# Optimization experiments

Hardware: AMD Instinct MI355X
Metric: run time of the kernel (lower is better)

## Reference

```python
import jax, jax.numpy as jnp
import numpy as np

BATCH, IN_DIM, OUT_DIM, DEGREE = 4096, 1024, 1024, 7


def setup_inputs() -> dict:
    key = jax.random.key(0)
    k1, k2 = jax.random.split(key)
    std = 1.0 / (IN_DIM * (DEGREE + 1))
    return {
        "x": jax.random.normal(k1, (BATCH, IN_DIM), dtype=jnp.float32),
        "a": jnp.zeros((1,), dtype=jnp.float32),
        "q": jnp.ones((1,), dtype=jnp.float32),
        "coeffs": jax.random.normal(k2, (IN_DIM, OUT_DIM, DEGREE + 1), dtype=jnp.float32) * std,
    }


def reference(x, a, q, coeffs):
    # x: [B, I]; a, q: [1]; coeffs: [I, O, D+1]
    xt = jnp.tanh(x)
    n_basis = coeffs.shape[-1]  # degree + 1
    # Iterative three-term recurrence (avoids the exponential naive recursion):
    # P0 = 1; P1 = x - a; Pn = (x - (a + q^n)) P_{n-1} - a q^{n-1} P_{n-2}
    basis = [jnp.ones_like(xt)]
    if n_basis > 1:
        basis.append(xt - a)
    for n in range(2, n_basis):
        pn = (xt - (a + q ** n)) * basis[-1] - a * (q ** (n - 1)) * basis[-2]
        basis.append(pn)
    B = jnp.stack(basis, axis=-1)  # [B, I, D+1]
    y = jnp.einsum('bid,iod->bo', B, coeffs)
    return y
```

## Files before the change

### kernel.cpp

```cpp
#include <hip/hip_runtime.h>

#define BATCH   4096
#define IN_DIM  1024
#define OUT_DIM 1024
#define NB      8
#define NBK     7
#define KD2     (IN_DIM * NBK)

typedef __bf16 bf16x8 __attribute__((ext_vector_type(8)));
typedef float  f32x4  __attribute__((ext_vector_type(4)));
typedef unsigned short us8 __attribute__((ext_vector_type(8)));
typedef unsigned short us4 __attribute__((ext_vector_type(4)));

__device__ __forceinline__ unsigned short f2bf(float f) {
    unsigned int u = __float_as_uint(f);
    u += 0x7fffu + ((u >> 16) & 1u);
    return (unsigned short)(u >> 16);
}

__device__ __forceinline__ float fast_tanh(float x) {
    const float LOG2E_X2 = 2.8853900817779268f;
    float e = __builtin_amdgcn_exp2f(x * LOG2E_X2);
    return 1.0f - 2.0f * __builtin_amdgcn_rcpf(e + 1.0f);
}

__device__ __forceinline__ void ld_lds16(const unsigned short* g, unsigned short* l) {
    __builtin_amdgcn_global_load_lds(
        (const __attribute__((address_space(1))) void*)g,
        (__attribute__((address_space(3))) void*)l, 16, 0, 0);
}

__device__ __forceinline__ unsigned lds_off(const void* p) {
    return (unsigned)(unsigned long long)
        (const __attribute__((address_space(3))) void*)p;
}

template <int OFF>
__device__ __forceinline__ bf16x8 dsr128(unsigned addr) {
    f32x4 r;
    asm volatile("ds_read_b128 %0, %1 offset:%c2"
                 : "=v"(r) : "v"(addr), "i"(OFF));
    union { f32x4 f; bf16x8 h; } u; u.f = r; return u.h;
}

#define PREP_BLOCKS   BATCH
#define REPACK_BLOCKS 512
#define ZERO_BLOCKS   (BATCH * OUT_DIM / 4096)
#define TI 32
#define TO 64
#define RSTR 232

__global__ __launch_bounds__(256) void prep_and_repack(
    const float* __restrict__ x, const float* __restrict__ ap,
    const float* __restrict__ qp, const float* __restrict__ coeffs,
    unsigned short* __restrict__ Aw, unsigned short* __restrict__ Bt,
    float* __restrict__ bias_part,
    float* __restrict__ C) {
    __shared__ __align__(16) unsigned short lt[TO * RSTR + 512];
    const int tid = threadIdx.x;

    if (blockIdx.x < PREP_BLOCKS) {
        const int b = blockIdx.x;
        const float a = ap[0], q = qp[0];
        float4 xv = *(const float4*)(x + (size_t)b * IN_DIM + tid * 4);
        float xe[4] = {xv.x, xv.y, xv.z, xv.w};
        float pm2[4], pm1[4];
        us4 ov;
#pragma unroll
        for (int e = 0; e < 4; ++e) {
            xe[e] = fast_tanh(xe[e]);
            pm2[e] = 1.0f;
            pm1[e] = xe[e] - a;
            ov[e] = f2bf(pm1[e]);
        }
        unsigned short* arow = Aw + (size_t)b * KD2 + tid * 4;
        *(us4*)arow = ov;
        float qn = q, qn1 = 1.0f;
#pragma unroll
        for (int n = 2; n < NB; ++n) {
            qn *= q; qn1 *= q;
#pragma unroll
            for (int e = 0; e < 4; ++e) {
                float pn = (xe[e] - (a + qn)) * pm1[e] - a * qn1 * pm2[e];
                pm2[e] = pm1[e]; pm1[e] = pn;
                ov[e] = f2bf(pn);
            }
            *(us4*)(arow + (size_t)(n - 1) * IN_DIM) = ov;
        }
        return;
    }

    const int bid = blockIdx.x - PREP_BLOCKS;
    if (bid < REPACK_BLOCKS) {
        const int g  = bid & 31;
        const int i0 = g * TI;
        const int o0 = (bid >> 5) * TO;
        const int o_local = tid & 63;
        float bpart = 0.f;
#pragma unroll
        for (int pass = 0; pass < 8; ++pass) {
            const int i_local = pass * 4 + (tid >> 6);
            const float* src = coeffs +
                ((size_t)(i0 + i_local) * OUT_DIM + (o0 + o_local)) * NB;
            float4 v0 = *(const float4*)src;
            float4 v1 = *(const float4*)(src + 4);
            bpart += v0.x;
            unsigned short* dst = lt + o_local * RSTR + i_local;
            dst[0]   = f2bf(v0.y); dst[32]  = f2bf(v0.z); dst[64]  = f2bf(v0.w);
            dst[96]  = f2bf(v1.x); dst[128] = f2bf(v1.y); dst[160] = f2bf(v1.z);
            dst[192] = f2bf(v1.w);
        }
        float* sb = (float*)(lt + TO * RSTR);
        sb[(tid >> 6) * 64 + o_local] = bpart;
        __syncthreads();
        if (tid < 64)
            bias_part[(size_t)g * OUT_DIM + o0 + tid] =
                sb[tid] + sb[64 + tid] + sb[128 + tid] + sb[192 + tid];
#pragma unroll
        for (int p = 0; p < 7; ++p) {
            const int o = tid >> 2;
            const int c = tid & 3;
            us8 v = *(const us8*)(lt + o * RSTR + p * 32 + c * 8);
            *(us8*)(Bt + (size_t)(o0 + o) * KD2 + (size_t)p * IN_DIM + i0 + c * 8) = v;
        }
        return;
    }

    const int z = bid - REPACK_BLOCKS;
    float* dst = C + (size_t)z * 4096 + tid * 4;
    const f32x4 zero = {0.f, 0.f, 0.f, 0.f};
#pragma unroll
    for (int j = 0; j < 4; ++j) *(f32x4*)(dst + j * 1024) = zero;
}

#define BM2 256
#define BN2 256
#define BK2 64
#define KSPLIT 4
#define KCH (KD2 / KSPLIT)
#define NT  (KCH / BK2)
#define GEMM_LDS 131072

#define ISSUE_A(TT_, SL_, L_)                                                  \
    ld_lds16(gA + (size_t)(L_) * 64 * KD2 +                                    \
                 (size_t)((TT_) < NT ? (TT_) : (NT - 1)) * 64,                 \
             lds + (SL_) * 16384 + (L_) * 4096 + tid * 8)

#define ISSUE_B(TT_, SL_, L_)                                                  \
    ld_lds16(gB + (size_t)(L_) * 64 * KD2 +                                    \
                 (size_t)((TT_) < NT ? (TT_) : (NT - 1)) * 64,                 \
             lds + 32768 + (SL_) * 16384 + (L_) * 4096 + tid * 8)

#define BARRIER_A()                                                            \
    __builtin_amdgcn_s_barrier();                                              \
    asm volatile("s_waitcnt lgkmcnt(0)" ::: "memory");                         \
    __builtin_amdgcn_sched_barrier(0);

#define MFMA16(M_, A0_, A1_, A2_, A3_)                                         \
    __builtin_amdgcn_s_setprio(1);                                             \
    _Pragma("unroll") for (int nf = 0; nf < 4; ++nf) {                         \
        acc[M_][nf] = __builtin_amdgcn_mfma_f32_16x16x32_bf16(                 \
            A0_, bF[nf][0], acc[M_][nf], 0, 0, 0);                             \
        acc[M_][nf] = __builtin_amdgcn_mfma_f32_16x16x32_bf16(                 \
            A1_, bF[nf][1], acc[M_][nf], 0, 0, 0);                             \
        acc[(M_) + 1][nf] = __builtin_amdgcn_mfma_f32_16x16x32_bf16(           \
            A2_, bF[nf][0], acc[(M_) + 1][nf], 0, 0, 0);                       \
        acc[(M_) + 1][nf] = __builtin_amdgcn_mfma_f32_16x16x32_bf16(           \
            A3_, bF[nf][1], acc[(M_) + 1][nf], 0, 0, 0);                       \
    }                                                                          \
    __builtin_amdgcn_s_setprio(0);                                             \
    __builtin_amdgcn_sched_barrier(0);

#define TILE_BODY(T_, P_)                                                      \
    {                                                                          \
        constexpr int OFF = (P_) * 32768;                                      \
        {                                                    \
            bf16x8 a0 = dsr128<OFF>(aA[0]), a1 = dsr128<OFF>(aA[0] ^ 64);      \
            bf16x8 a2 = dsr128<OFF>(aA[1]), a3 = dsr128<OFF>(aA[1] ^ 64);      \
            _Pragma("unroll") for (int nf = 0; nf < 4; ++nf) {                 \
                bF[nf][0] = dsr128<OFF>(bA[nf]);                               \
                bF[nf][1] = dsr128<OFF>(bA[nf] ^ 64);                          \
            }                                                                  \
            ISSUE_A((T_) + 1, (P_) ^ 1, 1);                                    \
            ISSUE_A((T_) + 1, (P_) ^ 1, 3);                                    \
            BARRIER_A()                                                        \
            MFMA16(0, a0, a1, a2, a3)                                          \
            __builtin_amdgcn_s_barrier();                                      \
        }                                                                      \
        {                                                    \
            bf16x8 a0 = dsr128<OFF>(aA[2]), a1 = dsr128<OFF>(aA[2] ^ 64);      \
            bf16x8 a2 = dsr128<OFF>(aA[3]), a3 = dsr128<OFF>(aA[3] ^ 64);      \
            ISSUE_B((T_) + 2, (P_), 0);                                        \
            ISSUE_B((T_) + 2, (P_), 1);                                        \
            BARRIER_A()                                                        \
            MFMA16(2, a0, a1, a2, a3)                                          \
            asm volatile("s_waitcnt vmcnt(10)" ::: "memory");                  \
            __builtin_amdgcn_s_barrier();                                      \
        }                                                                      \
        {                                                    \
            bf16x8 a0 = dsr128<OFF>(aA[4]), a1 = dsr128<OFF>(aA[4] ^ 64);      \
            bf16x8 a2 = dsr128<OFF>(aA[5]), a3 = dsr128<OFF>(aA[5] ^ 64);      \
            ISSUE_B((T_) + 2, (P_), 2);                                        \
            ISSUE_B((T_) + 2, (P_), 3);                                        \
            BARRIER_A()                                                        \
            MFMA16(4, a0, a1, a2, a3)                                          \
            __builtin_amdgcn_s_barrier();                                      \
        }                                                                      \
        {                                                    \
            bf16x8 a0 = dsr128<OFF>(aA[6]), a1 = dsr128<OFF>(aA[6] ^ 64);      \
            bf16x8 a2 = dsr128<OFF>(aA[7]), a3 = dsr128<OFF>(aA[7] ^ 64);      \
            ISSUE_A((T_) + 2, (P_), 0);                                        \
            ISSUE_A((T_) + 2, (P_), 2);                                        \
            BARRIER_A()                                                        \
            MFMA16(6, a0, a1, a2, a3)                                          \
            asm volatile("s_waitcnt vmcnt(8)" ::: "memory");                   \
            __builtin_amdgcn_s_barrier();                                      \
        }                                                                      \
    }

__global__ __launch_bounds__(512, 2) void gemm_kernel(
    const unsigned short* __restrict__ A,
    const unsigned short* __restrict__ Bt,
    const float* __restrict__ bias_part,
    float* __restrict__ C) {
    extern __shared__ __align__(16) unsigned short lds[];

    const int tid  = threadIdx.x;
    const int bidx = blockIdx.x;
    const int xcd = bidx & 7;
    const int g   = bidx >> 3;
    const int m0 = (xcd * 2 + (g & 1)) * BM2;
    const int n0 = ((g >> 1) & 3) * BN2;
    const int ch = g >> 3;
    const size_t kb = (size_t)ch * KCH;

    const int lane  = tid & 63;
    const int w     = tid >> 6;
    const int wmG   = (w >> 2) * 128;
    const int wnG   = (w & 3) * 64;
    const int row16 = lane & 15;
    const int quad  = lane >> 4;

    const unsigned ldsb = lds_off(lds);
    unsigned aA[8], bA[4];
#pragma unroll
    for (int mf = 0; mf < 8; ++mf) {
        int r = wmG + mf * 16 + row16;
        aA[mf] = ldsb + 2u * (unsigned)(r * 64 + ((quad ^ (r & 7)) * 8));
    }
#pragma unroll
    for (int nf = 0; nf < 4; ++nf) {
        int c = wnG + nf * 16 + row16;
        bA[nf] = ldsb + 65536u + 2u * (unsigned)(c * 64 + ((quad ^ (c & 7)) * 8));
    }

    const int rst = tid >> 3;
    const int sw  = ((tid & 7) ^ (rst & 7)) * 8;
    const unsigned short* gA = A  + (size_t)(m0 + rst) * KD2 + kb + sw;
    const unsigned short* gB = Bt + (size_t)(n0 + rst) * KD2 + kb + sw;

    f32x4  acc[8][4] = {};
    bf16x8 bF[4][2];

    ISSUE_B(0, 0, 0); ISSUE_B(0, 0, 1); ISSUE_B(0, 0, 2); ISSUE_B(0, 0, 3);
    ISSUE_A(0, 0, 0); ISSUE_A(0, 0, 2);
    ISSUE_A(0, 0, 1); ISSUE_A(0, 0, 3);
    ISSUE_B(1, 1, 0); ISSUE_B(1, 1, 1); ISSUE_B(1, 1, 2); ISSUE_B(1, 1, 3);
    ISSUE_A(1, 1, 0); ISSUE_A(1, 1, 2);
    asm volatile("s_waitcnt vmcnt(8)" ::: "memory");
    __builtin_amdgcn_s_barrier();

#pragma unroll 1
    for (int t = 0; t < NT; t += 2) {
        TILE_BODY(t, 0)
        TILE_BODY(t + 1, 1)
    }

    asm volatile("s_waitcnt vmcnt(0)" ::: "memory");
    __syncthreads();

    float* sbf = (float*)lds;
    if (ch == 0) {
        if (tid < 256) {
            float s = 0.f;
#pragma unroll
            for (int gg = 0; gg < 32; ++gg)
                s += bias_part[(size_t)gg * OUT_DIM + n0 + tid];
            sbf[tid] = s;
        }
        __syncthreads();
    }

#pragma unroll
    for (int mf = 0; mf < 8; ++mf) {
        const int rbase = m0 + wmG + mf * 16 + quad * 4;
#pragma unroll
        for (int nf = 0; nf < 4; ++nf) {
            const int col = n0 + wnG + nf * 16 + row16;
            const float bv = (ch == 0) ? sbf[wnG + nf * 16 + row16] : 0.f;
#pragma unroll
            for (int r = 0; r < 4; ++r)
                atomicAdd(&C[(size_t)(rbase + r) * OUT_DIM + col],
                          acc[mf][nf][r] + bv);
        }
    }
}

__global__ __launch_bounds__(256) void fallback_kernel(
    const float* __restrict__ x, const float* __restrict__ ap,
    const float* __restrict__ qp, const float* __restrict__ coeffs,
    float* __restrict__ out) {
    __shared__ float sb[IN_DIM][NB];
    const int b = blockIdx.x;
    const float a = ap[0], q = qp[0];
    for (int i = threadIdx.x; i < IN_DIM; i += 256) {
        float xt = fast_tanh(x[(size_t)b * IN_DIM + i]);
        float p0 = 1.0f, p1 = xt - a;
        sb[i][0] = p0; sb[i][1] = p1;
        float qn = q, qn1 = 1.0f;
#pragma unroll
        for (int n = 2; n < NB; ++n) {
            qn *= q; qn1 *= q;
            float p2 = (xt - (a + qn)) * p1 - a * qn1 * p0;
            sb[i][n] = p2;
            p0 = p1; p1 = p2;
        }
    }
    __syncthreads();
    float acc[4] = {0.f, 0.f, 0.f, 0.f};
    for (int i = 0; i < IN_DIM; ++i) {
        float bb[NB];
#pragma unroll
        for (int d = 0; d < NB; ++d) bb[d] = sb[i][d];
#pragma unroll
        for (int j = 0; j < 4; ++j) {
            int o = threadIdx.x + j * 256;
            const float* cf = coeffs + ((size_t)i * OUT_DIM + o) * NB;
            float s = 0.f;
#pragma unroll
            for (int d = 0; d < NB; ++d) s += bb[d] * cf[d];
            acc[j] += s;
        }
    }
#pragma unroll
    for (int j = 0; j < 4; ++j)
        out[(size_t)b * OUT_DIM + threadIdx.x + j * 256] = acc[j];
}

extern "C" void kernel_launch(void* const* d_in, const int* in_sizes, int n_in,
                              void* d_out, int out_size, void* d_ws, size_t ws_size,
                              hipStream_t stream) {
    const float* x      = (const float*)d_in[0];
    const float* a      = (const float*)d_in[1];
    const float* q      = (const float*)d_in[2];
    const float* coeffs = (const float*)d_in[3];
    float* out = (float*)d_out;

    const size_t needA = (size_t)BATCH * KD2 * sizeof(unsigned short);
    const size_t needB = (size_t)OUT_DIM * KD2 * sizeof(unsigned short);
    const size_t needBias = 32 * (size_t)OUT_DIM * sizeof(float);

    if (ws_size >= needA + needB + needBias) {
        static bool lds_attr_set = false;
        if (!lds_attr_set) {
            (void)hipFuncSetAttribute(
                reinterpret_cast<const void*>(&gemm_kernel),
                hipFuncAttributeMaxDynamicSharedMemorySize, GEMM_LDS);
            lds_attr_set = true;
        }
        unsigned short* Aw = (unsigned short*)d_ws;
        unsigned short* Bt = Aw + (size_t)BATCH * KD2;
        float* bias_part = (float*)((char*)d_ws + needA + needB);
        prep_and_repack<<<PREP_BLOCKS + REPACK_BLOCKS + ZERO_BLOCKS, 256, 0, stream>>>(
            x, a, q, coeffs, Aw, Bt, bias_part, out);
        gemm_kernel<<<(BATCH / BM2) * (OUT_DIM / BN2) * KSPLIT, 512, GEMM_LDS, stream>>>(
            Aw, Bt, bias_part, out);
    } else {
        fallback_kernel<<<BATCH, 256, 0, stream>>>(x, a, q, coeffs, out);
    }
}
```

Baseline: 200.2 us.

## Replace split-K atomics with partial buffers and a separate reduce kernel

The split-K GEMM now writes each K-chunk's partial result with plain stores, chunk 0 into the output and the others into workspace buffers. A new reduce kernel then sums them, which removes both the zeroing pass and the fp32 atomics. The block-to-XCD mapping now keeps each K-chunk on a pair of XCDs, the basis prep handles 8 elements per thread, and an atomic-based smaller-tile GEMM is added as a fallback when workspace is short. This trades atomic traffic for an extra 48 MB of partial writes plus a fourth kernel launch that reads them back.

Measured after the change: 168.2 us. -16.0%, faster.

```diff
diff --git a/kernel.cpp b/kernel.cpp
--- a/kernel.cpp
+++ b/kernel.cpp
@@ -43,55 +43,23 @@
     union { f32x4 f; bf16x8 h; } u; u.f = r; return u.h;
 }
 
-#define PREP_BLOCKS   BATCH
 #define REPACK_BLOCKS 512
-#define ZERO_BLOCKS   (BATCH * OUT_DIM / 4096)
+#define BASIS_BLOCKS  (BATCH / 2)
+#define PREP_BLOCKS   (REPACK_BLOCKS + BASIS_BLOCKS)
 #define TI 32
 #define TO 64
 #define RSTR 232
 
-__global__ __launch_bounds__(256) void prep_and_repack(
+__global__ __launch_bounds__(256) void prep_kernel(
     const float* __restrict__ x, const float* __restrict__ ap,
     const float* __restrict__ qp, const float* __restrict__ coeffs,
     unsigned short* __restrict__ Aw, unsigned short* __restrict__ Bt,
-    float* __restrict__ bias_part,
-    float* __restrict__ C) {
+    float* __restrict__ bias_part) {
     __shared__ __align__(16) unsigned short lt[TO * RSTR + 512];
     const int tid = threadIdx.x;
 
-    if (blockIdx.x < PREP_BLOCKS) {
-        const int b = blockIdx.x;
-        const float a = ap[0], q = qp[0];
-        float4 xv = *(const float4*)(x + (size_t)b * IN_DIM + tid * 4);
-        float xe[4] = {xv.x, xv.y, xv.z, xv.w};
-        float pm2[4], pm1[4];
-        us4 ov;
-#pragma unroll
-        for (int e = 0; e < 4; ++e) {
-            xe[e] = fast_tanh(xe[e]);
-            pm2[e] = 1.0f;
-            pm1[e] = xe[e] - a;
-            ov[e] = f2bf(pm1[e]);
-        }
-        unsigned short* arow = Aw + (size_t)b * KD2 + tid * 4;
-        *(us4*)arow = ov;
-        float qn = q, qn1 = 1.0f;
-#pragma unroll
-        for (int n = 2; n < NB; ++n) {
-            qn *= q; qn1 *= q;
-#pragma unroll
-            for (int e = 0; e < 4; ++e) {
-                float pn = (xe[e] - (a + qn)) * pm1[e] - a * qn1 * pm2[e];
-                pm2[e] = pm1[e]; pm1[e] = pn;
-                ov[e] = f2bf(pn);
-            }
-            *(us4*)(arow + (size_t)(n - 1) * IN_DIM) = ov;
-        }
-        return;
-    }
-
-    const int bid = blockIdx.x - PREP_BLOCKS;
-    if (bid < REPACK_BLOCKS) {
+    if (blockIdx.x < REPACK_BLOCKS) {
+        const int bid = blockIdx.x;
         const int g  = bid & 31;
         const int i0 = g * TI;
         const int o0 = (bid >> 5) * TO;
@@ -126,18 +94,56 @@
         return;
     }
 
-    const int z = bid - REPACK_BLOCKS;
-    float* dst = C + (size_t)z * 4096 + tid * 4;
+    const int bb  = blockIdx.x - REPACK_BLOCKS;
+    const float a = ap[0], q = qp[0];
+    const int b  = bb * 2 + (tid >> 7);
+    const int i0 = (tid & 127) * 8;
+
+    const float* xs = x + (size_t)b * IN_DIM + i0;
+    float4 v0 = *(const float4*)xs;
+    float4 v1 = *(const float4*)(xs + 4);
+
+    float xe[8] = {v0.x, v0.y, v0.z, v0.w, v1.x, v1.y, v1.z, v1.w};
+    float pm2[8], pm1[8];
+    us8 ov;
+#pragma unroll
+    for (int e = 0; e < 8; ++e) {
+        xe[e] = fast_tanh(xe[e]);
+        pm2[e] = 1.0f;
+        pm1[e] = xe[e] - a;
+        ov[e] = f2bf(pm1[e]);
+    }
+    unsigned short* arow = Aw + (size_t)b * KD2 + i0;
+    *(us8*)arow = ov;
+    float qn = q, qn1 = 1.0f;
+#pragma unroll
+    for (int n = 2; n < NB; ++n) {
+        qn *= q; qn1 *= q;
+#pragma unroll
+        for (int e = 0; e < 8; ++e) {
+            float pn = (xe[e] - (a + qn)) * pm1[e] - a * qn1 * pm2[e];
+            pm2[e] = pm1[e]; pm1[e] = pn;
+            ov[e] = f2bf(pn);
+        }
+        *(us8*)(arow + (size_t)(n - 1) * IN_DIM) = ov;
+    }
+}
+
+#define ZERO_BLOCKS   (BATCH * OUT_DIM / 4096)
+
+__global__ __launch_bounds__(256) void zero_kernel(float* __restrict__ C) {
+    float* dst = C + (size_t)blockIdx.x * 4096 + threadIdx.x * 4;
     const f32x4 zero = {0.f, 0.f, 0.f, 0.f};
 #pragma unroll
     for (int j = 0; j < 4; ++j) *(f32x4*)(dst + j * 1024) = zero;
 }
+
+#define KSPLIT 4
+#define KCH (KD2 / KSPLIT)
 
 #define BM2 256
 #define BN2 256
 #define BK2 64
-#define KSPLIT 4
-#define KCH (KD2 / KSPLIT)
 #define NT  (KCH / BK2)
 #define GEMM_LDS 131072
 
@@ -218,20 +224,22 @@
         }                                                                      \
     }
 
-__global__ __launch_bounds__(512, 2) void gemm_kernel(
+__global__ __launch_bounds__(512, 2) void gemm8_store(
     const unsigned short* __restrict__ A,
     const unsigned short* __restrict__ Bt,
     const float* __restrict__ bias_part,
+    float* __restrict__ Cp,
     float* __restrict__ C) {
     extern __shared__ __align__(16) unsigned short lds[];
 
     const int tid  = threadIdx.x;
     const int bidx = blockIdx.x;
-    const int xcd = bidx & 7;
-    const int g   = bidx >> 3;
-    const int m0 = (xcd * 2 + (g & 1)) * BM2;
-    const int n0 = ((g >> 1) & 3) * BN2;
-    const int ch = g >> 3;
+    const int xcd   = bidx & 7;
+    const int ch    = xcd >> 1;
+    const int mhalf = xcd & 1;
+    const int loc   = bidx >> 3;
+    const int m0 = ((loc >> 2) + mhalf * 8) * BM2;
+    const int n0 = (loc & 3) * BN2;
     const size_t kb = (size_t)ch * KCH;
 
     const int lane  = tid & 63;
@@ -291,6 +299,7 @@
         __syncthreads();
     }
 
+    float* dst = (ch == 0) ? C : (Cp + (size_t)(ch - 1) * BATCH * OUT_DIM);
 #pragma unroll
     for (int mf = 0; mf < 8; ++mf) {
         const int rbase = m0 + wmG + mf * 16 + quad * 4;
@@ -300,9 +309,117 @@
             const float bv = (ch == 0) ? sbf[wnG + nf * 16 + row16] : 0.f;
 #pragma unroll
             for (int r = 0; r < 4; ++r)
-                atomicAdd(&C[(size_t)(rbase + r) * OUT_DIM + col],
-                          acc[mf][nf][r] + bv);
-        }
+                dst[(size_t)(rbase + r) * OUT_DIM + col] = acc[mf][nf][r] + bv;
+        }
+    }
+}
+
+#define BM 128
+#define BN 128
+#define BK 64
+
+__global__ __launch_bounds__(256, 4) void gemm_atomic(
+    const unsigned short* __restrict__ A,
+    const unsigned short* __restrict__ Bt,
+    const float* __restrict__ bias_part,
+    float* __restrict__ C) {
+    __shared__ __align__(16) unsigned short lA[BM * BK];
+    __shared__ __align__(16) unsigned short lB[BN * BK];
+    const int tid  = threadIdx.x;
+    const int bidx = blockIdx.x;
+    const int ch    = (bidx & 7) >> 1;
+    const int mhalf = bidx & 1;
+    const int loc   = bidx >> 3;
+    const int m0 = ((loc >> 3) + mhalf * 16) * BM;
+    const int n0 = (loc & 7) * BN;
+    const size_t kb = (size_t)ch * KCH;
+    const int lane  = tid & 63;
+    const int wid   = tid >> 6;
+    const int wm    = (wid & 1) * 64;
+    const int wn    = (wid >> 1) * 64;
+    const int row16 = lane & 15;
+    const int quad  = lane >> 4;
+    int aOff[4], bOff[4];
+#pragma unroll
+    for (int mt = 0; mt < 4; ++mt) {
+        int r = wm + mt * 16 + row16;
+        aOff[mt] = r * BK + ((quad ^ (r & 7)) * 8);
+    }
+#pragma unroll
+    for (int nt = 0; nt < 4; ++nt) {
+        int c = wn + nt * 16 + row16;
+        bOff[nt] = c * BK + ((quad ^ (c & 7)) * 8);
+    }
+    const int r0 = tid >> 3, s0 = tid & 7;
+    const unsigned short* gA0 = A  + (size_t)(m0 + r0) * KD2 + kb + ((s0 ^ (r0 & 7)) * 8);
+    const unsigned short* gB0 = Bt + (size_t)(n0 + r0) * KD2 + kb + ((s0 ^ (r0 & 7)) * 8);
+    unsigned short* dA = lA + tid * 8;
+    unsigned short* dB = lB + tid * 8;
+    f32x4 acc[4][4] = {};
+    for (int k0 = 0; k0 < KCH; k0 += BK) {
+#pragma unroll
+        for (int j = 0; j < 4; ++j)
+            ld_lds16(gA0 + k0 + (size_t)j * 32 * KD2, dA + j * 2048);
+#pragma unroll
+        for (int j = 0; j < 4; ++j)
+            ld_lds16(gB0 + k0 + (size_t)j * 32 * KD2, dB + j * 2048);
+        __syncthreads();
+#pragma unroll
+        for (int kk = 0; kk < 2; ++kk) {
+            const int xo = kk * 32;
+            bf16x8 aF[4], bF[4];
+#pragma unroll
+            for (int mt = 0; mt < 4; ++mt) aF[mt] = *(const bf16x8*)(lA + (aOff[mt] ^ xo));
+#pragma unroll
+            for (int nt = 0; nt < 4; ++nt) bF[nt] = *(const bf16x8*)(lB + (bOff[nt] ^ xo));
+#pragma unroll
+            for (int mt = 0; mt < 4; ++mt)
+#pragma unroll
+                for (int nt = 0; nt < 4; ++nt)
+                    acc[mt][nt] = __builtin_amdgcn_mfma_f32_16x16x32_bf16(
+                        aF[mt], bF[nt], acc[mt][nt], 0, 0, 0);
+        }
+        __syncthreads();
+    }
+    if (ch == 0) {
+        float* sbw = (float*)lA;
+        if (tid < BN) {
+            float s = 0.f;
+#pragma unroll
+            for (int g = 0; g < 32; ++g) s += bias_part[(size_t)g * OUT_DIM + n0 + tid];
+            sbw[tid] = s;
+        }
+        __syncthreads();
+    }
+    const float* sb = (const float*)lA;
+#pragma unroll
+    for (int mt = 0; mt < 4; ++mt) {
+        const int rbase = m0 + wm + mt * 16 + quad * 4;
+#pragma unroll
+        for (int nt = 0; nt < 4; ++nt) {
+            const int col = n0 + wn + nt * 16 + row16;
+            const float bv = (ch == 0) ? sb[wn + nt * 16 + row16] : 0.f;
+#pragma unroll
+            for (int r = 0; r < 4; ++r)
+                atomicAdd(&C[(size_t)(rbase + r) * OUT_DIM + col], acc[mt][nt][r] + bv);
+        }
+    }
+}
+
+__global__ __launch_bounds__(256) void reduce_kernel(
+    const float* __restrict__ Cp,
+    float* __restrict__ C) {
+    const size_t P = (size_t)BATCH * OUT_DIM;
+    const size_t base = (size_t)blockIdx.x * 4096 + threadIdx.x * 4;
+#pragma unroll
+    for (int j = 0; j < 4; ++j) {
+        const size_t idx = base + (size_t)j * 1024;
+        f32x4 v  = *(const f32x4*)(C + idx);
+        f32x4 v1 = *(const f32x4*)(Cp + idx);
+        f32x4 v2 = *(const f32x4*)(Cp + P + idx);
+        f32x4 v3 = *(const f32x4*)(Cp + 2 * P + idx);
+        v = v + v1 + v2 + v3;
+        *(f32x4*)(C + idx) = v;
     }
 }
 
@@ -359,21 +476,33 @@
     const size_t needA = (size_t)BATCH * KD2 * sizeof(unsigned short);
     const size_t needB = (size_t)OUT_DIM * KD2 * sizeof(unsigned short);
     const size_t needBias = 32 * (size_t)OUT_DIM * sizeof(float);
-
-    if (ws_size >= needA + needB + needBias) {
+    const size_t needCp = 3 * (size_t)BATCH * OUT_DIM * sizeof(float);
+
+    if (ws_size >= needA + needB + needBias + needCp) {
         static bool lds_attr_set = false;
         if (!lds_attr_set) {
             (void)hipFuncSetAttribute(
-                reinterpret_cast<const void*>(&gemm_kernel),
+                reinterpret_cast<const void*>(&gemm8_store),
                 hipFuncAttributeMaxDynamicSharedMemorySize, GEMM_LDS);
             lds_attr_set = true;
         }
         unsigned short* Aw = (unsigned short*)d_ws;
         unsigned short* Bt = Aw + (size_t)BATCH * KD2;
         float* bias_part = (float*)((char*)d_ws + needA + needB);
-        prep_and_repack<<<PREP_BLOCKS + REPACK_BLOCKS + ZERO_BLOCKS, 256, 0, stream>>>(
-            x, a, q, coeffs, Aw, Bt, bias_part, out);
-        gemm_kernel<<<(BATCH / BM2) * (OUT_DIM / BN2) * KSPLIT, 512, GEMM_LDS, stream>>>(
+        float* Cp = (float*)((char*)d_ws + needA + needB + needBias);
+        prep_kernel<<<PREP_BLOCKS, 256, 0, stream>>>(
+            x, a, q, coeffs, Aw, Bt, bias_part);
+        gemm8_store<<<(BATCH / BM2) * (OUT_DIM / BN2) * KSPLIT, 512, GEMM_LDS,
+                      stream>>>(Aw, Bt, bias_part, Cp, out);
+        reduce_kernel<<<BATCH * OUT_DIM / 4096, 256, 0, stream>>>(Cp, out);
+    } else if (ws_size >= needA + needB + needBias) {
+        unsigned short* Aw = (unsigned short*)d_ws;
+        unsigned short* Bt = Aw + (size_t)BATCH * KD2;
+        float* bias_part = (float*)((char*)d_ws + needA + needB);
+        prep_kernel<<<PREP_BLOCKS, 256, 0, stream>>>(
+            x, a, q, coeffs, Aw, Bt, bias_part);
+        zero_kernel<<<ZERO_BLOCKS, 256, 0, stream>>>(out);
+        gemm_atomic<<<(BATCH / BM) * (OUT_DIM / BN) * KSPLIT, 256, 0, stream>>>(
             Aw, Bt, bias_part, out);
     } else {
         fallback_kernel<<<BATCH, 256, 0, stream>>>(x, a, q, coeffs, out);
```
